# Optimization experiments

Hardware: AMD Instinct MI355X
Metric: run time of the kernel (lower is better)

The kernel has to match this reference:

```python
import jax, jax.numpy as jnp
import numpy as np

N_OBJ, P, M, D = 8, 65536, 32, 128


def setup_inputs() -> dict:
    key = jax.random.key(0)
    k1, k2, k3 = jax.random.split(key, 3)
    net_out = jax.random.normal(k1, (N_OBJ * P, D), dtype=jnp.float32)
    # cumulative end offsets per object; last entry (unused by the loop) repeats N_total
    pt_offset = jnp.concatenate([
        jnp.arange(1, N_OBJ + 1, dtype=jnp.int32) * P,
        jnp.array([N_OBJ * P], dtype=jnp.int32),
    ])
    mask_pts = jax.random.randint(k2, (N_OBJ, M, P), 0, 2, dtype=jnp.int32)
    mask_embs = jax.random.normal(k3, (N_OBJ * M, D), dtype=jnp.float32)
    logit_scale = jnp.ones((1,), dtype=jnp.float32)
    return {
        "net_out": net_out,
        "pt_offset": pt_offset,
        "mask_embs": mask_embs,
        "mask_pts": mask_pts,
        "logit_scale": logit_scale,
    }


def reference(net_out, pt_offset, mask_embs, mask_pts, logit_scale):
    # Uniform segments: object o owns points [o*P, (o+1)*P), matching pt_offset.
    n_obj, n_masks, n_pts = mask_pts.shape
    d = net_out.shape[1]
    x = net_out[: n_obj * n_pts].reshape(n_obj, n_pts, d)          # [O,P,D]
    emb = jnp.nan_to_num(
        mask_embs.reshape(n_obj, n_masks, d), nan=0.0, posinf=0.0, neginf=0.0
    )                                                               # [O,M,D]
    m = mask_pts.astype(net_out.dtype)                              # [O,M,P]

    # sum_p mask * ||x_p - e||^2 = sum_p m*||x_p||^2 + cnt*||e||^2 - 2 e . (sum_p m x_p)
    cnt = jnp.sum(m, axis=-1)                                       # [O,M]
    xsq = jnp.sum(x * x, axis=-1)                                   # [O,P]
    t1 = jnp.einsum("omp,op->om", m, xsq)                          # [O,M]
    t2 = cnt * jnp.sum(emb * emb, axis=-1)                          # [O,M]
    mx = jnp.einsum("omp,opd->omd", m, x)                          # [O,M,D]
    t3 = 2.0 * jnp.sum(emb * mx, axis=-1)                           # [O,M]

    sum_sq = jnp.sum(t1 + t2 - t3)
    total_points = jnp.sum(cnt)
    # torch: sum over masks of MSE(masked_pts, label)*n_pts, divided by total points
    # MSE*n_pts = sum_sq_per_mask / D; empty masks contribute 0 to both terms.
    return jnp.where(total_points > 0, sum_sq / (d * total_points), 0.0)
```

## Files before the change

### kernel.cpp

```cpp
#include <hip/hip_runtime.h>
#include <math.h>

#define NOBJ 8
#define NP   65536
#define NM   32
#define ND   128
#define CHUNKS 64
#define PTS_WG 1024
#define PTS_WAVE 256

__launch_bounds__(256, 2)
__global__ void distill_main(const float* __restrict__ net,
                             const float* __restrict__ embs,
                             const int* __restrict__ mask,
                             float* __restrict__ ws) {
  __shared__ float T[8 * 16 * ND];
  __shared__ float esq[NM];
  __shared__ int   Wlds[4 * PTS_WAVE];
  __shared__ float red[4][4];

  const int tid  = threadIdx.x;
  const int wave = tid >> 6;
  const int lane = tid & 63;
  const int bid  = blockIdx.x;
  const int o     = bid >> 6;
  const int chunk = bid & (CHUNKS - 1);

  const float* EB = embs + (size_t)o * NM * ND;

  if (tid < NM) {
    float a = 0.f;
    const float* e = EB + (size_t)tid * ND;
    for (int d_ = 0; d_ < ND; ++d_) {
      float v = e[d_];
      if (!isfinite(v)) v = 0.f;
      a += v * v;
    }
    esq[tid] = a;
  }

  for (int j = 0; j < 64; ++j) {
    int idx = j * 256 + tid;
    int d_ = idx & (ND - 1);
    int n  = (idx >> 7) & 15;
    int g  = idx >> 11;
    float acc = 0.f;
#pragma unroll
    for (int b = 0; b < 4; ++b) {
      if ((n >> b) & 1) {
        float e = EB[(size_t)(g * 4 + b) * ND + d_];
        if (!isfinite(e)) e = 0.f;
        acc += e;
      }
    }
    T[idx] = acc;
  }
  __syncthreads();

  const int p0 = chunk * PTS_WG + wave * PTS_WAVE;
  const int* mp = mask + (size_t)o * NM * NP + p0 + 4 * lane;
  int W0 = 0, W1 = 0, W2 = 0, W3 = 0;
  float pB = 0.f, TPl = 0.f;
#pragma unroll
  for (int m = 0; m < NM; ++m) {
    const int4 v = *(const int4*)(mp + (size_t)m * NP);
    int b0 = (v.x != 0), b1 = (v.y != 0), b2 = (v.z != 0), b3 = (v.w != 0);
    W0 |= b0 << m; W1 |= b1 << m; W2 |= b2 << m; W3 |= b3 << m;
    float c = (float)(b0 + b1 + b2 + b3);
    TPl += c;
    pB  += esq[m] * c;
  }
  *(int4*)&Wlds[wave * PTS_WAVE + 4 * lane] = make_int4(W0, W1, W2, W3);
  __syncthreads();

  const float* xo = net + ((size_t)o * NP + p0) * ND;
  const int half = lane >> 5;
  const int dl   = (lane & 31) * 4;
  float accA = 0.f, accC = 0.f;

  int    Wc = Wlds[wave * PTS_WAVE + half];
  float4 Xc = *(const float4*)(xo + (size_t)half * ND + dl);

  for (int i = 0; i < PTS_WAVE; i += 2) {
    int Wn = Wc; float4 Xn = Xc;
    if (i + 2 < PTS_WAVE) {
      Wn = Wlds[wave * PTS_WAVE + i + 2 + half];
      Xn = *(const float4*)(xo + (size_t)(i + 2 + half) * ND + dl);
    }

    float sq = Xc.x * Xc.x + Xc.y * Xc.y + Xc.z * Xc.z + Xc.w * Xc.w;
    accA += (float)__popc(Wc) * sq;

    float s0 = 0.f, s1 = 0.f, s2 = 0.f, s3 = 0.f;
#pragma unroll
    for (int g = 0; g < 8; ++g) {
      int n = (Wc >> (g * 4)) & 15;
      const float4 t = *(const float4*)&T[(g * 16 + n) * ND + dl];
      s0 += t.x; s1 += t.y; s2 += t.z; s3 += t.w;
    }
    accC += s0 * Xc.x + s1 * Xc.y + s2 * Xc.z + s3 * Xc.w;

    Wc = Wn; Xc = Xn;
  }

#pragma unroll
  for (int off = 32; off >= 1; off >>= 1) {
    accA += __shfl_xor(accA, off, 64);
    accC += __shfl_xor(accC, off, 64);
    pB   += __shfl_xor(pB,   off, 64);
    TPl  += __shfl_xor(TPl,  off, 64);
  }
  if (lane == 0) {
    red[wave][0] = accA; red[wave][1] = pB;
    red[wave][2] = accC; red[wave][3] = TPl;
  }
  __syncthreads();
  if (tid == 0) {
    float A = 0.f, B = 0.f, C = 0.f, TP = 0.f;
    for (int w = 0; w < 4; ++w) {
      A += red[w][0]; B += red[w][1]; C += red[w][2]; TP += red[w][3];
    }
    atomicAdd(&ws[0], A);
    atomicAdd(&ws[1], B);
    atomicAdd(&ws[2], C);
    atomicAdd(&ws[3], TP);
  }
}

__global__ void distill_final(const float* __restrict__ ws, float* __restrict__ out) {
  float A = ws[0], B = ws[1], C = ws[2], TP = ws[3];
  out[0] = (TP > 0.f) ? (A + B - 2.f * C) / ((float)ND * TP) : 0.f;
}

extern "C" void kernel_launch(void* const* d_in, const int* in_sizes, int n_in,
                              void* d_out, int out_size, void* d_ws, size_t ws_size,
                              hipStream_t stream) {
  const float* net  = (const float*)d_in[0];
  const float* embs = (const float*)d_in[2];
  const int*   mask = (const int*)d_in[3];
  float* ws = (float*)d_ws;

  hipMemsetAsync(d_ws, 0, 4 * sizeof(float), stream);
  distill_main<<<NOBJ * CHUNKS, 256, 0, stream>>>(net, embs, mask, ws);
  distill_final<<<1, 1, 0, stream>>>(ws, (float*)d_out);
}
```

Before: 454.6 us.

## Compute mask-embedding dot products with bf16 MFMA instead of LDS subset-sum tables

Replaces the LDS subset-sum lookup table approach with a direct per-point dot product of X against all 32 embeddings using 32x32x16 bf16 MFMA, then weights each result by the mask value. Mask and point loads are read straight from global memory with register prefetching, and the work split moves to 128 chunks per object with higher occupancy. This aims to remove the LDS-bound table accumulation, at the cost of bf16 rounding of inputs in the cross term, which may affect accuracy.

```diff
diff --git a/kernel.cpp b/kernel.cpp
--- a/kernel.cpp
+++ b/kernel.cpp
@@ -5,131 +5,126 @@
 #define NP   65536
 #define NM   32
 #define ND   128
-#define CHUNKS 64
-#define PTS_WG 1024
-#define PTS_WAVE 256
 
-__launch_bounds__(256, 2)
+typedef __attribute__((ext_vector_type(8)))  short short8;
+typedef __attribute__((ext_vector_type(16))) float f32x16;
+
+__device__ __forceinline__ short f2bf(float f) {
+  unsigned u = __float_as_uint(f);
+  return (short)((u + 0x7FFFu + ((u >> 16) & 1u)) >> 16);
+}
+
+__launch_bounds__(256, 4)
 __global__ void distill_main(const float* __restrict__ net,
                              const float* __restrict__ embs,
                              const int* __restrict__ mask,
                              float* __restrict__ ws) {
-  __shared__ float T[8 * 16 * ND];
-  __shared__ float esq[NM];
-  __shared__ int   Wlds[4 * PTS_WAVE];
-  __shared__ float red[4][4];
+  __shared__ float red[4][2];
 
   const int tid  = threadIdx.x;
   const int wave = tid >> 6;
   const int lane = tid & 63;
-  const int bid  = blockIdx.x;
-  const int o     = bid >> 6;
-  const int chunk = bid & (CHUNKS - 1);
+  const int row  = lane & 31;
+  const int h    = lane >> 5;
+  const int o     = blockIdx.x >> 7;
+  const int chunk = blockIdx.x & 127;
+  const int pbase = chunk * 512 + wave * 128;
 
-  const float* EB = embs + (size_t)o * NM * ND;
+  const float* X = net  + (size_t)o * NP * ND;
+  const float* E = embs + (size_t)o * NM * ND;
 
-  if (tid < NM) {
-    float a = 0.f;
-    const float* e = EB + (size_t)tid * ND;
-    for (int d_ = 0; d_ < ND; ++d_) {
-      float v = e[d_];
+  short8 Bf[8];
+  float esqp = 0.f;
+  const float* erow = E + (size_t)row * ND + 8 * h;
+#pragma unroll
+  for (int kk = 0; kk < 8; ++kk) {
+    float4 e0 = *(const float4*)(erow + 16 * kk);
+    float4 e1 = *(const float4*)(erow + 16 * kk + 4);
+    float ev[8] = {e0.x, e0.y, e0.z, e0.w, e1.x, e1.y, e1.z, e1.w};
+    short8 b;
+#pragma unroll
+    for (int j = 0; j < 8; ++j) {
+      float v = ev[j];
       if (!isfinite(v)) v = 0.f;
-      a += v * v;
+      esqp += v * v;
+      b[j] = f2bf(v);
     }
-    esq[tid] = a;
+    Bf[kk] = b;
+  }
+  const float esq = esqp + __shfl_xor(esqp, 32, 64);
+
+  auto ldx = [&](int t, int kk, float4& a, float4& b) {
+    const float* p = X + (size_t)(pbase + 32 * t + row) * ND + 8 * h + 16 * kk;
+    a = *(const float4*)p;
+    b = *(const float4*)(p + 4);
+  };
+
+  float4 r0[4], r1[4];
+#pragma unroll
+  for (int s = 0; s < 4; ++s) ldx(0, s, r0[s], r1[s]);
+
+  float S = 0.f, Cnt = 0.f;
+  for (int t = 0; t < 4; ++t) {
+    const int* mrow = mask + ((size_t)o * NM + row) * NP + pbase + 32 * t + 4 * h;
+    const int4 m0 = *(const int4*)(mrow);
+    const int4 m1 = *(const int4*)(mrow + 8);
+    const int4 m2 = *(const int4*)(mrow + 16);
+    const int4 m3 = *(const int4*)(mrow + 24);
+
+    f32x16 acc;
+#pragma unroll
+    for (int i = 0; i < 16; ++i) acc[i] = 0.f;
+    float xsqp = 0.f;
+
+#pragma unroll
+    for (int kk = 0; kk < 8; ++kk) {
+      float4 c0 = r0[kk & 3], c1 = r1[kk & 3];
+      if (kk < 4)      ldx(t, kk + 4, r0[kk & 3], r1[kk & 3]);
+      else if (t < 3)  ldx(t + 1, kk - 4, r0[kk & 3], r1[kk & 3]);
+
+      xsqp += c0.x * c0.x + c0.y * c0.y + c0.z * c0.z + c0.w * c0.w
+            + c1.x * c1.x + c1.y * c1.y + c1.z * c1.z + c1.w * c1.w;
+
+      short8 a;
+      a[0] = f2bf(c0.x); a[1] = f2bf(c0.y); a[2] = f2bf(c0.z); a[3] = f2bf(c0.w);
+      a[4] = f2bf(c1.x); a[5] = f2bf(c1.y); a[6] = f2bf(c1.z); a[7] = f2bf(c1.w);
+      acc = __builtin_amdgcn_mfma_f32_32x32x16_bf16(a, Bf[kk], acc, 0, 0, 0);
+    }
+
+    const float xsq = xsqp + __shfl_xor(xsqp, 32, 64);
+    const int mk[16] = {m0.x, m0.y, m0.z, m0.w, m1.x, m1.y, m1.z, m1.w,
+                        m2.x, m2.y, m2.z, m2.w, m3.x, m3.y, m3.z, m3.w};
+#pragma unroll
+    for (int reg = 0; reg < 16; ++reg) {
+      const int rowi = (reg & 3) + 8 * (reg >> 2) + 4 * h;
+      const float xr = __shfl(xsq, rowi, 64);
+      const float q  = acc[reg];
+      const float bitf = (float)mk[reg];
+      S   += bitf * (xr - 2.f * q);
+      Cnt += bitf;
+    }
   }
 
-  for (int j = 0; j < 64; ++j) {
-    int idx = j * 256 + tid;
-    int d_ = idx & (ND - 1);
-    int n  = (idx >> 7) & 15;
-    int g  = idx >> 11;
-    float acc = 0.f;
-#pragma unroll
-    for (int b = 0; b < 4; ++b) {
-      if ((n >> b) & 1) {
-        float e = EB[(size_t)(g * 4 + b) * ND + d_];
-        if (!isfinite(e)) e = 0.f;
-        acc += e;
-      }
-    }
-    T[idx] = acc;
-  }
-  __syncthreads();
-
-  const int p0 = chunk * PTS_WG + wave * PTS_WAVE;
-  const int* mp = mask + (size_t)o * NM * NP + p0 + 4 * lane;
-  int W0 = 0, W1 = 0, W2 = 0, W3 = 0;
-  float pB = 0.f, TPl = 0.f;
-#pragma unroll
-  for (int m = 0; m < NM; ++m) {
-    const int4 v = *(const int4*)(mp + (size_t)m * NP);
-    int b0 = (v.x != 0), b1 = (v.y != 0), b2 = (v.z != 0), b3 = (v.w != 0);
-    W0 |= b0 << m; W1 |= b1 << m; W2 |= b2 << m; W3 |= b3 << m;
-    float c = (float)(b0 + b1 + b2 + b3);
-    TPl += c;
-    pB  += esq[m] * c;
-  }
-  *(int4*)&Wlds[wave * PTS_WAVE + 4 * lane] = make_int4(W0, W1, W2, W3);
-  __syncthreads();
-
-  const float* xo = net + ((size_t)o * NP + p0) * ND;
-  const int half = lane >> 5;
-  const int dl   = (lane & 31) * 4;
-  float accA = 0.f, accC = 0.f;
-
-  int    Wc = Wlds[wave * PTS_WAVE + half];
-  float4 Xc = *(const float4*)(xo + (size_t)half * ND + dl);
-
-  for (int i = 0; i < PTS_WAVE; i += 2) {
-    int Wn = Wc; float4 Xn = Xc;
-    if (i + 2 < PTS_WAVE) {
-      Wn = Wlds[wave * PTS_WAVE + i + 2 + half];
-      Xn = *(const float4*)(xo + (size_t)(i + 2 + half) * ND + dl);
-    }
-
-    float sq = Xc.x * Xc.x + Xc.y * Xc.y + Xc.z * Xc.z + Xc.w * Xc.w;
-    accA += (float)__popc(Wc) * sq;
-
-    float s0 = 0.f, s1 = 0.f, s2 = 0.f, s3 = 0.f;
-#pragma unroll
-    for (int g = 0; g < 8; ++g) {
-      int n = (Wc >> (g * 4)) & 15;
-      const float4 t = *(const float4*)&T[(g * 16 + n) * ND + dl];
-      s0 += t.x; s1 += t.y; s2 += t.z; s3 += t.w;
-    }
-    accC += s0 * Xc.x + s1 * Xc.y + s2 * Xc.z + s3 * Xc.w;
-
-    Wc = Wn; Xc = Xn;
-  }
-
+  float val = S + esq * Cnt;
+  float tp  = Cnt;
 #pragma unroll
   for (int off = 32; off >= 1; off >>= 1) {
-    accA += __shfl_xor(accA, off, 64);
-    accC += __shfl_xor(accC, off, 64);
-    pB   += __shfl_xor(pB,   off, 64);
-    TPl  += __shfl_xor(TPl,  off, 64);
+    val += __shfl_xor(val, off, 64);
+    tp  += __shfl_xor(tp,  off, 64);
   }
-  if (lane == 0) {
-    red[wave][0] = accA; red[wave][1] = pB;
-    red[wave][2] = accC; red[wave][3] = TPl;
-  }
+  if (lane == 0) { red[wave][0] = val; red[wave][1] = tp; }
   __syncthreads();
   if (tid == 0) {
-    float A = 0.f, B = 0.f, C = 0.f, TP = 0.f;
-    for (int w = 0; w < 4; ++w) {
-      A += red[w][0]; B += red[w][1]; C += red[w][2]; TP += red[w][3];
-    }
-    atomicAdd(&ws[0], A);
-    atomicAdd(&ws[1], B);
-    atomicAdd(&ws[2], C);
-    atomicAdd(&ws[3], TP);
+    float a = red[0][0] + red[1][0] + red[2][0] + red[3][0];
+    float b = red[0][1] + red[1][1] + red[2][1] + red[3][1];
+    atomicAdd(&ws[0], a);
+    atomicAdd(&ws[1], b);
   }
 }
 
 __global__ void distill_final(const float* __restrict__ ws, float* __restrict__ out) {
-  float A = ws[0], B = ws[1], C = ws[2], TP = ws[3];
-  out[0] = (TP > 0.f) ? (A + B - 2.f * C) / ((float)ND * TP) : 0.f;
+  float sum_sq = ws[0], tp = ws[1];
+  out[0] = (tp > 0.f) ? sum_sq / ((float)ND * tp) : 0.f;
 }
 
 extern "C" void kernel_launch(void* const* d_in, const int* in_sizes, int n_in,
@@ -141,6 +136,6 @@
   float* ws = (float*)d_ws;
 
   hipMemsetAsync(d_ws, 0, 4 * sizeof(float), stream);
-  distill_main<<<NOBJ * CHUNKS, 256, 0, stream>>>(net, embs, mask, ws);
+  distill_main<<<NOBJ * 128, 256, 0, stream>>>(net, embs, mask, ws);
   distill_final<<<1, 1, 0, stream>>>(ws, (float*)d_out);
 }
```

Result: faster. 432.8 us (-4.8%).
